# Optimization experiments

Measured on AMD Instinct MI355X. Metric: run time of the kernel, lower is better.

## Reference

```python
import jax, jax.numpy as jnp
import numpy as np

EPS = 1e-8  # torch CosineSimilarity eps


def _cosine_sim_matrix(x, y):
    # x: [Nx, D], y: [Ny, D] -> [Nx, Ny] cosine similarity via normalized GEMM
    xn = x / jnp.maximum(jnp.linalg.norm(x, axis=-1, keepdims=True), EPS)
    yn = y / jnp.maximum(jnp.linalg.norm(y, axis=-1, keepdims=True), EPS)
    return xn @ yn.T


def setup_inputs() -> dict:
    key = jax.random.key(0)
    k1, k2, k3, k4 = jax.random.split(key, 4)
    N, D, C = 4096, 512, 100
    inst_embed = jax.random.normal(k1, (N, D), dtype=jnp.float32)
    proxy = jax.random.normal(k2, (N, D), dtype=jnp.float32)
    # binary positive-selection mask per class over the batch
    negative_mask = (jax.random.uniform(k3, (C, N)) > 0.5).astype(jnp.float32)
    labels = jax.random.randint(k4, (N,), 0, C, dtype=jnp.int64)
    temperature = jnp.float32(0.1)
    margin = jnp.float32(0.0)
    return {"inst_embed": inst_embed, "proxy": proxy,
            "negative_mask": negative_mask, "labels": labels,
            "temperature": temperature, "margin": margin}


def reference(inst_embed, proxy, negative_mask, labels, temperature, margin):
    # [N, N] similarity matrices
    p2i = _cosine_sim_matrix(proxy, inst_embed)
    i2i = _cosine_sim_matrix(inst_embed, inst_embed)
    p2i_zone = jnp.exp((p2i - margin) / temperature)
    i2i_zone = jnp.exp((i2i - margin) / temperature)
    mask = negative_mask[labels]  # [N, N]
    p2i_num = (p2i_zone * mask).sum(axis=1)
    i2i_num = (i2i_zone * mask).sum(axis=1)
    p2i_den = p2i_zone.sum(axis=1)
    i2i_den = i2i_zone.sum(axis=1)
    p2i_loss = -jnp.log(temperature * (p2i_num / p2i_den)).mean()
    i2i_loss = -jnp.log(temperature * (i2i_num / i2i_den)).mean()
    return p2i_loss + i2i_loss
```

## Files before the change

kernel.cpp:

```cpp
#include <hip/hip_runtime.h>
#include <hip/hip_bf16.h>

#define D_DIM 512
#define KSTEPS 16
#define BM 64
#define BN 64
#define GRIDY 4

typedef __bf16 bf16x8 __attribute__((ext_vector_type(8)));
typedef float  f32x4  __attribute__((ext_vector_type(4)));

__device__ __forceinline__ unsigned short f2bf_rne(float x) {
    unsigned int u = __float_as_uint(x);
    u += 0x7FFFu + ((u >> 16) & 1u);
    return (unsigned short)(u >> 16);
}

__global__ __launch_bounds__(128) void normalize_rows(
    const float* __restrict__ inst, const float* __restrict__ proxy,
    unsigned short* __restrict__ instb, unsigned short* __restrict__ proxyb, int N)
{
    int row = blockIdx.x;
    const float* src;
    unsigned short* dst;
    if (row < N) { src = inst  + (size_t)row * D_DIM;        dst = instb  + (size_t)row * D_DIM; }
    else         { src = proxy + (size_t)(row - N) * D_DIM;  dst = proxyb + (size_t)(row - N) * D_DIM; }
    int t = threadIdx.x;
    float4 v = ((const float4*)src)[t];
    float ss = v.x*v.x + v.y*v.y + v.z*v.z + v.w*v.w;
    #pragma unroll
    for (int off = 32; off > 0; off >>= 1) ss += __shfl_down(ss, off, 64);
    __shared__ float wss[2];
    if ((t & 63) == 0) wss[t >> 6] = ss;
    __syncthreads();
    float inv = 1.0f / fmaxf(sqrtf(wss[0] + wss[1]), 1e-8f);
    ushort4 o;
    o.x = f2bf_rne(v.x * inv); o.y = f2bf_rne(v.y * inv);
    o.z = f2bf_rne(v.z * inv); o.w = f2bf_rne(v.w * inv);
    ((ushort4*)dst)[t] = o;
}

__global__ __launch_bounds__(256, 2) void fused_scores(
    const unsigned short* __restrict__ instb,
    const unsigned short* __restrict__ proxyb,
    const float* __restrict__ negmask,
    const int*  __restrict__ labels,
    const float* __restrict__ temp_p,
    const float* __restrict__ margin_p,
    float* __restrict__ nd,
    int N, int colsPerBlock)
{
    __shared__ unsigned short Bt[BN * D_DIM];

    const int tid  = threadIdx.x;
    const int lane = tid & 63;
    const int wave = tid >> 6;
    const int quad = lane >> 4;
    const int l16  = lane & 15;

    const int Rbase  = blockIdx.x * BM + wave * 16;
    const bool isP2I = (Rbase < N);
    const unsigned short* Aptr = isP2I ? (proxyb + (size_t)Rbase * D_DIM)
                                       : (instb  + (size_t)(Rbase - N) * D_DIM);
    const int rowLocal = isP2I ? Rbase : (Rbase - N);

    const float temp  = *temp_p;
    const float scale = 1.44269504088896340736f / temp;
    const float bias  = -(*margin_p) * scale;

    bf16x8 Afrag[KSTEPS];
    {
        const unsigned short* arow = Aptr + (size_t)l16 * D_DIM + quad * 8;
        #pragma unroll
        for (int ks = 0; ks < KSTEPS; ks++)
            Afrag[ks] = *(const bf16x8*)(arow + ks * 32);
    }

    int lab[4];
    #pragma unroll
    for (int r = 0; r < 4; r++) lab[r] = labels[rowLocal + quad * 4 + r];

    float numAcc[4] = {0.f,0.f,0.f,0.f};
    float denAcc[4] = {0.f,0.f,0.f,0.f};

    const int j0base = blockIdx.y * colsPerBlock;
    for (int jt = 0; jt < colsPerBlock; jt += BN) {
        const int j0 = j0base + jt;
        __syncthreads();
        #pragma unroll
        for (int it = 0; it < (BN * (D_DIM/8)) / 256; it++) {
            int c   = tid + it * 256;
            int br  = c >> 6;
            int ch  = c & 63;
            int chs = ch ^ (br & 7);
            float4 v = ((const float4*)(instb + (size_t)(j0 + br) * D_DIM))[ch];
            *(float4*)&Bt[br * D_DIM + chs * 8] = v;
        }
        __syncthreads();

        f32x4 acc[4] = {};
        #pragma unroll
        for (int ks = 0; ks < KSTEPS; ks++) {
            #pragma unroll
            for (int cg = 0; cg < 4; cg++) {
                int rB  = cg * 16 + l16;
                int chs = (ks * 4 + quad) ^ (rB & 7);
                bf16x8 b = *(const bf16x8*)&Bt[rB * D_DIM + chs * 8];
                acc[cg] = __builtin_amdgcn_mfma_f32_16x16x32_bf16(Afrag[ks], b, acc[cg], 0, 0, 0);
            }
        }

        #pragma unroll
        for (int cg = 0; cg < 4; cg++) {
            int j = j0 + cg * 16 + l16;
            #pragma unroll
            for (int r = 0; r < 4; r++) {
                float zone = exp2f(acc[cg][r] * scale + bias);
                denAcc[r] += zone;
                float m = negmask[(size_t)lab[r] * N + j];
                numAcc[r] += zone * m;
            }
        }
    }

    #pragma unroll
    for (int r = 0; r < 4; r++) {
        float n = numAcc[r], d = denAcc[r];
        #pragma unroll
        for (int off = 8; off > 0; off >>= 1) {
            n += __shfl_down(n, off, 16);
            d += __shfl_down(d, off, 16);
        }
        if (l16 == 0) {
            float* numArr = nd + (isP2I ? 0 : 2 * N);
            float* denArr = numArr + N;
            atomicAdd(&numArr[rowLocal + quad * 4 + r], n);
            atomicAdd(&denArr[rowLocal + quad * 4 + r], d);
        }
    }
}

__global__ __launch_bounds__(256) void loss_reduce(
    const float* __restrict__ nd, const float* __restrict__ temp_p,
    float* __restrict__ out, int N)
{
    const float t = *temp_p;
    float s = 0.f;
    for (int i = threadIdx.x; i < N; i += 256) {
        s -= logf(t * nd[i]         / nd[N + i]);
        s -= logf(t * nd[2 * N + i] / nd[3 * N + i]);
    }
    #pragma unroll
    for (int off = 32; off > 0; off >>= 1) s += __shfl_down(s, off, 64);
    __shared__ float wss[4];
    if ((threadIdx.x & 63) == 0) wss[threadIdx.x >> 6] = s;
    __syncthreads();
    if (threadIdx.x == 0) out[0] = (wss[0] + wss[1] + wss[2] + wss[3]) / (float)N;
}

extern "C" void kernel_launch(void* const* d_in, const int* in_sizes, int n_in,
                              void* d_out, int out_size, void* d_ws, size_t ws_size,
                              hipStream_t stream)
{
    const float* inst     = (const float*)d_in[0];
    const float* proxy    = (const float*)d_in[1];
    const float* negmask  = (const float*)d_in[2];
    const int*   labels   = (const int*)d_in[3];
    const float* temp_p   = (const float*)d_in[4];
    const float* margin_p = (const float*)d_in[5];
    float* out = (float*)d_out;

    const int N = in_sizes[3];

    unsigned short* instb  = (unsigned short*)d_ws;
    unsigned short* proxyb = instb + (size_t)N * D_DIM;
    float* nd = (float*)(proxyb + (size_t)N * D_DIM);

    hipMemsetAsync(nd, 0, sizeof(float) * 4 * N, stream);
    normalize_rows<<<2 * N, 128, 0, stream>>>(inst, proxy, instb, proxyb, N);
    dim3 grid(2 * N / BM, GRIDY);
    fused_scores<<<grid, 256, 0, stream>>>(instb, proxyb, negmask, labels,
                                           temp_p, margin_p, nd, N, N / GRIDY);
    loss_reduce<<<1, 256, 0, stream>>>(nd, temp_p, out, N);
}
```

Baseline: 143.6 us.

## Share B tiles between p2i and i2i rows, use direct global-to-LDS loads

```diff
diff --git a/kernel.cpp b/kernel.cpp
--- a/kernel.cpp
+++ b/kernel.cpp
@@ -5,7 +5,7 @@
 #define KSTEPS 16
 #define BM 64
 #define BN 64
-#define GRIDY 4
+#define GRIDY 8
 
 typedef __bf16 bf16x8 __attribute__((ext_vector_type(8)));
 typedef float  f32x4  __attribute__((ext_vector_type(4)));
@@ -14,6 +14,12 @@
     unsigned int u = __float_as_uint(x);
     u += 0x7FFFu + ((u >> 16) & 1u);
     return (unsigned short)(u >> 16);
+}
+
+__device__ __forceinline__ void g2l16(const void* g, void* l) {
+    __builtin_amdgcn_global_load_lds(
+        (const __attribute__((address_space(1))) unsigned int*)g,
+        (__attribute__((address_space(3))) unsigned int*)l, 16, 0, 0);
 }
 
 __global__ __launch_bounds__(128) void normalize_rows(
@@ -58,104 +64,111 @@
     const int quad = lane >> 4;
     const int l16  = lane & 15;
 
-    const int Rbase  = blockIdx.x * BM + wave * 16;
-    const bool isP2I = (Rbase < N);
-    const unsigned short* Aptr = isP2I ? (proxyb + (size_t)Rbase * D_DIM)
-                                       : (instb  + (size_t)(Rbase - N) * D_DIM);
-    const int rowLocal = isP2I ? Rbase : (Rbase - N);
+    const int row0 = blockIdx.x * BM + wave * 16;
 
     const float temp  = *temp_p;
     const float scale = 1.44269504088896340736f / temp;
     const float bias  = -(*margin_p) * scale;
 
-    bf16x8 Afrag[KSTEPS];
+    bf16x8 Ap[KSTEPS], Ai[KSTEPS];
     {
-        const unsigned short* arow = Aptr + (size_t)l16 * D_DIM + quad * 8;
+        const unsigned short* pr = proxyb + (size_t)(row0 + l16) * D_DIM + quad * 8;
+        const unsigned short* ir = instb  + (size_t)(row0 + l16) * D_DIM + quad * 8;
         #pragma unroll
-        for (int ks = 0; ks < KSTEPS; ks++)
-            Afrag[ks] = *(const bf16x8*)(arow + ks * 32);
+        for (int ks = 0; ks < KSTEPS; ks++) {
+            Ap[ks] = *(const bf16x8*)(pr + ks * 32);
+            Ai[ks] = *(const bf16x8*)(ir + ks * 32);
+        }
     }
 
     int lab[4];
     #pragma unroll
-    for (int r = 0; r < 4; r++) lab[r] = labels[rowLocal + quad * 4 + r];
+    for (int r = 0; r < 4; r++) lab[r] = labels[row0 + quad * 4 + r];
 
-    float numAcc[4] = {0.f,0.f,0.f,0.f};
-    float denAcc[4] = {0.f,0.f,0.f,0.f};
+    float numP[4] = {0.f,0.f,0.f,0.f}, denP[4] = {0.f,0.f,0.f,0.f};
+    float numI[4] = {0.f,0.f,0.f,0.f}, denI[4] = {0.f,0.f,0.f,0.f};
 
     const int j0base = blockIdx.y * colsPerBlock;
     for (int jt = 0; jt < colsPerBlock; jt += BN) {
         const int j0 = j0base + jt;
         __syncthreads();
         #pragma unroll
-        for (int it = 0; it < (BN * (D_DIM/8)) / 256; it++) {
-            int c   = tid + it * 256;
-            int br  = c >> 6;
-            int ch  = c & 63;
-            int chs = ch ^ (br & 7);
-            float4 v = ((const float4*)(instb + (size_t)(j0 + br) * D_DIM))[ch];
-            *(float4*)&Bt[br * D_DIM + chs * 8] = v;
+        for (int it = 0; it < (BN * (D_DIM / 8)) / 256; it++) {
+            const int br = it * 4 + wave;
+            const unsigned short* src =
+                instb + (size_t)(j0 + br) * D_DIM + ((lane ^ (br & 7)) * 8);
+            g2l16(src, &Bt[(size_t)(it * 256 + wave * 64) * 8]);
         }
         __syncthreads();
 
-        f32x4 acc[4] = {};
+        f32x4 accP[4] = {}, accI[4] = {};
         #pragma unroll
         for (int ks = 0; ks < KSTEPS; ks++) {
             #pragma unroll
             for (int cg = 0; cg < 4; cg++) {
-                int rB  = cg * 16 + l16;
-                int chs = (ks * 4 + quad) ^ (rB & 7);
-                bf16x8 b = *(const bf16x8*)&Bt[rB * D_DIM + chs * 8];
-                acc[cg] = __builtin_amdgcn_mfma_f32_16x16x32_bf16(Afrag[ks], b, acc[cg], 0, 0, 0);
+                const int rB  = cg * 16 + l16;
+                const int chs = (ks * 4 + quad) ^ (rB & 7);
+                bf16x8 b = *(const bf16x8*)&Bt[(size_t)rB * D_DIM + chs * 8];
+                accP[cg] = __builtin_amdgcn_mfma_f32_16x16x32_bf16(Ap[ks], b, accP[cg], 0, 0, 0);
+                accI[cg] = __builtin_amdgcn_mfma_f32_16x16x32_bf16(Ai[ks], b, accI[cg], 0, 0, 0);
             }
         }
 
         #pragma unroll
         for (int cg = 0; cg < 4; cg++) {
-            int j = j0 + cg * 16 + l16;
+            const int j = j0 + cg * 16 + l16;
             #pragma unroll
             for (int r = 0; r < 4; r++) {
-                float zone = exp2f(acc[cg][r] * scale + bias);
-                denAcc[r] += zone;
-                float m = negmask[(size_t)lab[r] * N + j];
-                numAcc[r] += zone * m;
+                const float m = negmask[(size_t)lab[r] * N + j];
+                float zp = exp2f(accP[cg][r] * scale + bias);
+                float zi = exp2f(accI[cg][r] * scale + bias);
+                denP[r] += zp; numP[r] += zp * m;
+                denI[r] += zi; numI[r] += zi * m;
             }
         }
     }
 
     #pragma unroll
     for (int r = 0; r < 4; r++) {
-        float n = numAcc[r], d = denAcc[r];
+        float np = numP[r], dp = denP[r], ni = numI[r], di = denI[r];
         #pragma unroll
         for (int off = 8; off > 0; off >>= 1) {
-            n += __shfl_down(n, off, 16);
-            d += __shfl_down(d, off, 16);
+            np += __shfl_down(np, off, 16);
+            dp += __shfl_down(dp, off, 16);
+            ni += __shfl_down(ni, off, 16);
+            di += __shfl_down(di, off, 16);
         }
         if (l16 == 0) {
-            float* numArr = nd + (isP2I ? 0 : 2 * N);
-            float* denArr = numArr + N;
-            atomicAdd(&numArr[rowLocal + quad * 4 + r], n);
-            atomicAdd(&denArr[rowLocal + quad * 4 + r], d);
+            const int row = row0 + quad * 4 + r;
+            atomicAdd(&nd[row],         np);
+            atomicAdd(&nd[N + row],     dp);
+            atomicAdd(&nd[2 * N + row], ni);
+            atomicAdd(&nd[3 * N + row], di);
         }
     }
 }
 
-__global__ __launch_bounds__(256) void loss_reduce(
+__global__ __launch_bounds__(1024) void loss_reduce(
     const float* __restrict__ nd, const float* __restrict__ temp_p,
     float* __restrict__ out, int N)
 {
     const float t = *temp_p;
     float s = 0.f;
-    for (int i = threadIdx.x; i < N; i += 256) {
-        s -= logf(t * nd[i]         / nd[N + i]);
-        s -= logf(t * nd[2 * N + i] / nd[3 * N + i]);
+    for (int i = threadIdx.x; i < N; i += 1024) {
+        s += (logf(nd[N + i])     - logf(nd[i]));
+        s += (logf(nd[3 * N + i]) - logf(nd[2 * N + i]));
     }
     #pragma unroll
     for (int off = 32; off > 0; off >>= 1) s += __shfl_down(s, off, 64);
-    __shared__ float wss[4];
+    __shared__ float wss[16];
     if ((threadIdx.x & 63) == 0) wss[threadIdx.x >> 6] = s;
     __syncthreads();
-    if (threadIdx.x == 0) out[0] = (wss[0] + wss[1] + wss[2] + wss[3]) / (float)N;
+    if (threadIdx.x < 16) {
+        float v = wss[threadIdx.x];
+        #pragma unroll
+        for (int off = 8; off > 0; off >>= 1) v += __shfl_down(v, off, 16);
+        if (threadIdx.x == 0) out[0] = v / (float)N - 2.0f * logf(t);
+    }
 }
 
 extern "C" void kernel_launch(void* const* d_in, const int* in_sizes, int n_in,
@@ -178,8 +191,8 @@
 
     hipMemsetAsync(nd, 0, sizeof(float) * 4 * N, stream);
     normalize_rows<<<2 * N, 128, 0, stream>>>(inst, proxy, instb, proxyb, N);
-    dim3 grid(2 * N / BM, GRIDY);
+    dim3 grid(N / BM, GRIDY);
     fused_scores<<<grid, 256, 0, stream>>>(instb, proxyb, negmask, labels,
                                            temp_p, margin_p, nd, N, N / GRIDY);
-    loss_reduce<<<1, 256, 0, stream>>>(nd, temp_p, out, N);
+    loss_reduce<<<1, 1024, 0, stream>>>(nd, temp_p, out, N);
 }
```

Measured after the change: 121.4 us. 1.18x faster.
